# Performance work log

Hardware: AMD Instinct MI355X
Metric: run time of the kernel (lower is better)

The kernel has to match this reference:

```python
import jax, jax.numpy as jnp
import numpy as np

B, S, N, F_RAW = 32, 48, 1000, 21
H = 64           # hidden_dim
A_DIM = 10       # aspect_dim
FEAT = 4 * A_DIM # projected feature_dim = 40

OFF_IDX = np.array([2, 5, 8, 9, 12])
DEF_IDX = np.array([10, 14, 15])
ERR_IDX = np.array([13, 17])
INF_IDX = np.array([19, 20])


def _glorot(k, shape):
    lim = (6.0 / (shape[0] + shape[1])) ** 0.5
    return jax.random.uniform(k, shape, minval=-lim, maxval=lim, dtype=jnp.float32)


def setup_inputs() -> dict:
    key = jax.random.key(0)
    ks = jax.random.split(key, 12)
    return {
        'inputs': jax.random.normal(ks[0], (B, S, N, F_RAW), dtype=jnp.float32),
        'adj': jax.random.uniform(ks[1], (N, N), dtype=jnp.float32),
        # aspect projection linears (weight stored as [in, out])
        'Wo': _glorot(ks[2], (5, A_DIM)), 'bo': jnp.zeros((A_DIM,), jnp.float32),
        'Wd': _glorot(ks[3], (3, A_DIM)), 'bd': jnp.zeros((A_DIM,), jnp.float32),
        'We': _glorot(ks[4], (2, A_DIM)), 'be': jnp.zeros((A_DIM,), jnp.float32),
        'Wi': _glorot(ks[5], (2, A_DIM)), 'bi': jnp.zeros((A_DIM,), jnp.float32),
        # graph-conv GRU weights: gates (bias init 1.0) and candidate (bias 0.0)
        'W1': _glorot(ks[6], (H + FEAT, 2 * H)), 'b1': jnp.ones((2 * H,), jnp.float32),
        'W2': _glorot(ks[7], (H + FEAT, H)), 'b2': jnp.zeros((H,), jnp.float32),
    }


def _laplacian_with_self_loop(adj):
    A = adj + jnp.eye(adj.shape[0], dtype=adj.dtype)
    d_inv_sqrt = A.sum(axis=1) ** -0.5
    return d_inv_sqrt[:, None] * A * d_inv_sqrt[None, :]


def reference(inputs, adj, Wo, bo, Wd, bd, We, be, Wi, bi, W1, b1, W2, b2):
    b, s, n, _ = inputs.shape
    L = _laplacian_with_self_loop(adj)  # [N, N]

    # vectorized per-node aspect projections -> [B, S, N, 40]
    x = jnp.concatenate([
        inputs[..., OFF_IDX] @ Wo + bo,
        inputs[..., DEF_IDX] @ Wd + bd,
        inputs[..., ERR_IDX] @ We + be,
        inputs[..., INF_IDX] @ Wi + bi,
    ], axis=-1)

    def gconv(x_t, h_flat, W, bias, out_dim):
        # x_t: [B, N, FEAT]; h_flat: [B, N*H]
        cat = jnp.concatenate([x_t, h_flat.reshape(b, n, H)], axis=-1)  # [B,N,H+FEAT]
        ag = jnp.einsum('mn,bnf->bmf', L, cat)                          # [B,N,H+FEAT]
        out = ag @ W + bias                                             # [B,N,out_dim]
        return out.reshape(b, n * out_dim)

    def step(h_flat, x_t):
        # NOTE: chunk over the flattened (B, N*2H) axis, as in the torch code
        ru = jax.nn.sigmoid(gconv(x_t, h_flat, W1, b1, 2 * H))  # [B, N*2H]
        r, u = jnp.split(ru, 2, axis=1)                          # each [B, N*H]
        c = jnp.tanh(gconv(x_t, r * h_flat, W2, b2, H))          # [B, N*H]
        h_new = u * h_flat + (1.0 - u) * c
        return h_new, None

    h0 = jnp.zeros((b, n * H), dtype=inputs.dtype)
    h_last, _ = jax.lax.scan(step, h0, jnp.swapaxes(x, 0, 1))  # scan over seq
    return h_last.reshape(b, n, H)
```

## Files before the change

### kernel.cpp

```cpp
#include <hip/hip_runtime.h>
#include <math.h>

#define NN    1000
#define KP    1024
#define BATCH 32
#define SEQ   48
#define HID   64
#define LCOLS 32256

typedef unsigned short u16;
typedef __attribute__((ext_vector_type(8))) short  short8v;
typedef __attribute__((ext_vector_type(8))) unsigned short ushort8v;
typedef __attribute__((ext_vector_type(4))) float  float4v;

__device__ __forceinline__ u16 f2bf(float x) {
    union { float f; unsigned u; } v; v.f = x;
    unsigned r = v.u + 0x7FFF + ((v.u >> 16) & 1);
    return (u16)(r >> 16);
}
__device__ __forceinline__ float bf2f(u16 h) {
    union { unsigned u; float f; } v; v.u = ((unsigned)h) << 16;
    return v.f;
}

__global__ void k_rowsum(const float* __restrict__ adj, float* __restrict__ dinv) {
    int m = blockIdx.x;
    float s = 0.f;
    for (int n = threadIdx.x; n < NN; n += blockDim.x)
        s += adj[(size_t)m*NN + n];
    __shared__ float red[256];
    red[threadIdx.x] = s; __syncthreads();
    for (int st = 128; st > 0; st >>= 1) {
        if (threadIdx.x < st) red[threadIdx.x] += red[threadIdx.x + st];
        __syncthreads();
    }
    if (threadIdx.x == 0) dinv[m] = rsqrtf(red[0] + 1.0f);
}

__global__ void k_buildL(const float* __restrict__ adj, const float* __restrict__ dinv,
                         u16* __restrict__ Lhi) {
    int idx = blockIdx.x * 256 + threadIdx.x;
    if (idx >= KP*KP) return;
    int m = idx >> 10, k = idx & (KP-1);
    float v = 0.f;
    if (m < NN && k < NN)
        v = dinv[m] * (adj[(size_t)m*NN + k] + (m == k ? 1.f : 0.f)) * dinv[k];
    Lhi[idx] = f2bf(v);
}

__global__ void k_buildLf(const float* __restrict__ adj, const float* __restrict__ dinv,
                          u16* __restrict__ Lf) {
    size_t idx = (size_t)blockIdx.x * 256 + threadIdx.x;
    if (idx >= (size_t)KP*KP) return;
    int e    = idx & 7;
    int lane = (idx >> 3) & 63;
    int kb   = (idx >> 9) & 31;
    int mg   = idx >> 14;
    int m = mg*16 + (lane & 15);
    int k = kb*32 + (lane >> 4)*8 + e;
    float v = 0.f;
    if (m < NN && k < NN)
        v = dinv[m] * (adj[(size_t)m*NN + k] + (m == k ? 1.f : 0.f)) * dinv[k];
    Lf[idx] = f2bf(v);
}

__global__ void k_srow(const float* __restrict__ adj, const float* __restrict__ dinv,
                       float* __restrict__ srl) {
    int m = blockIdx.x;
    __shared__ float red[256];
    float s = 0.f;
    if (m < NN)
        for (int n = threadIdx.x; n < NN; n += blockDim.x)
            s += adj[(size_t)m*NN + n] * dinv[n];
    red[threadIdx.x] = s; __syncthreads();
    for (int st = 128; st > 0; st >>= 1) {
        if (threadIdx.x < st) red[threadIdx.x] += red[threadIdx.x + st];
        __syncthreads();
    }
    if (threadIdx.x == 0) srl[m] = (m < NN) ? dinv[m] * (red[0] + dinv[m]) : 0.f;
}

__global__ void k_wconv(const float* __restrict__ W1, const float* __restrict__ W2,
                        u16* __restrict__ W1h, u16* __restrict__ W2h) {
    int idx = blockIdx.x * 256 + threadIdx.x;
    if (idx < 128*128) {
        int k = idx >> 7, f = idx & 127;
        W1h[idx] = f2bf((f < 104) ? W1[f*128 + k] : 0.f);
    } else if (idx < 128*128 + 64*128) {
        int i2 = idx - 128*128;
        int c = i2 >> 7, f = i2 & 127;
        W2h[i2] = f2bf((f < 104) ? W2[f*64 + c] : 0.f);
    }
}

__global__ void k_packW(const float* __restrict__ Wo, const float* __restrict__ bo,
                        const float* __restrict__ Wd, const float* __restrict__ bd,
                        const float* __restrict__ We, const float* __restrict__ be,
                        const float* __restrict__ Wi, const float* __restrict__ bi,
                        float* __restrict__ Wp, float* __restrict__ bp) {
    for (int o = threadIdx.x; o < 21*40; o += 256) {
        int f = o / 40, a = o - f*40;
        int g = a / 10, aa = a - 10*g;
        float v = 0.f;
        if (g == 0) {
            if (f == 2) v = Wo[0*10+aa]; else if (f == 5) v = Wo[1*10+aa];
            else if (f == 8) v = Wo[2*10+aa]; else if (f == 9) v = Wo[3*10+aa];
            else if (f == 12) v = Wo[4*10+aa];
        } else if (g == 1) {
            if (f == 10) v = Wd[aa]; else if (f == 14) v = Wd[10+aa];
            else if (f == 15) v = Wd[20+aa];
        } else if (g == 2) {
            if (f == 13) v = We[aa]; else if (f == 17) v = We[10+aa];
        } else {
            if (f == 19) v = Wi[aa]; else if (f == 20) v = Wi[10+aa];
        }
        Wp[o] = v;
    }
    if (threadIdx.x < 40) {
        int a = threadIdx.x, g = a / 10, aa = a - 10*g;
        bp[a] = (g == 0) ? bo[aa] : (g == 1) ? bd[aa] : (g == 2) ? be[aa] : bi[aa];
    }
}

__global__ __launch_bounds__(256)
void k_transpose(const float* __restrict__ inputs, u16* __restrict__ inT) {
    int bt = blockIdx.x;
    int b = bt / SEQ, t = bt - b*SEQ;
    int nt = blockIdx.y;
    __shared__ float sm[128][22];
    const float* base = inputs + ((size_t)bt * NN + nt*128) * 21;
    for (int i = threadIdx.x; i < 128*21; i += 256) {
        int nn = i / 21, f = i - nn*21;
        int n = nt*128 + nn;
        sm[nn][f] = (n < NN) ? base[(size_t)nn*21 + f] : 0.f;
    }
    __syncthreads();
    for (int o = threadIdx.x; o < 21*128; o += 256) {
        int f = o >> 7, nn = o & 127;
        inT[(size_t)((t*32 + b)*21 + f)*KP + nt*128 + nn] = f2bf(sm[nn][f]);
    }
}

__global__ __launch_bounds__(512)
void k_gemm(const u16* __restrict__ A, const u16* __restrict__ B,
            u16* __restrict__ Cout, int ncols) {
    __shared__ char sA[128*64];
    __shared__ char sB[64*64];
    const int n0 = blockIdx.x * 64;
    const int m0 = blockIdx.y * 128;
    const int tid = threadIdx.x;
    const int w = tid >> 6, lane = tid & 63;
    const int l15 = lane & 15, l4 = lane >> 4;
    const int wm = w >> 1, wn = w & 1;

    float4v acc[2][2];
    #pragma unroll
    for (int i = 0; i < 2; ++i)
        #pragma unroll
        for (int j = 0; j < 2; ++j) acc[i][j] = (float4v){0.f,0.f,0.f,0.f};

    int aoff[2], boff[2];
    #pragma unroll
    for (int mf = 0; mf < 2; ++mf) {
        int r = wm*32 + mf*16 + l15;
        aoff[mf] = (r*64 + l4*16) ^ ((r & 7) << 4);
    }
    #pragma unroll
    for (int nf = 0; nf < 2; ++nf) {
        int r = wn*32 + nf*16 + l15;
        boff[nf] = (r*64 + l4*16) ^ ((r & 7) << 4);
    }
    const int rA = tid >> 2, qA = tid & 3;
    const int dA = (rA*64 + qA*16) ^ ((rA & 7) << 4);
    const size_t gA = (size_t)(m0 + rA)*KP + qA*8;
    const int rB = (tid & 255) >> 2, qB = tid & 3;
    const int dB = (rB*64 + qB*16) ^ ((rB & 7) << 4);
    const size_t gB = (size_t)(n0 + rB)*KP + qB*8;

    for (int kt = 0; kt < 32; ++kt) {
        const int k0 = kt*32;
        __syncthreads();
        *(uint4*)(sA + dA) = *(const uint4*)(A + gA + k0);
        if (tid < 256) *(uint4*)(sB + dB) = *(const uint4*)(B + gB + k0);
        __syncthreads();
        short8v a0 = *(const short8v*)(sA + aoff[0]);
        short8v a1 = *(const short8v*)(sA + aoff[1]);
        short8v b0 = *(const short8v*)(sB + boff[0]);
        short8v b1 = *(const short8v*)(sB + boff[1]);
        acc[0][0] = __builtin_amdgcn_mfma_f32_16x16x32_bf16(a0, b0, acc[0][0], 0, 0, 0);
        acc[0][1] = __builtin_amdgcn_mfma_f32_16x16x32_bf16(a0, b1, acc[0][1], 0, 0, 0);
        acc[1][0] = __builtin_amdgcn_mfma_f32_16x16x32_bf16(a1, b0, acc[1][0], 0, 0, 0);
        acc[1][1] = __builtin_amdgcn_mfma_f32_16x16x32_bf16(a1, b1, acc[1][1], 0, 0, 0);
    }
    #pragma unroll
    for (int mf = 0; mf < 2; ++mf)
        #pragma unroll
        for (int nf = 0; nf < 2; ++nf)
            #pragma unroll
            for (int i = 0; i < 4; ++i) {
                int m = m0 + wm*32 + mf*16 + l4*4 + i;
                int j = n0 + wn*32 + nf*16 + l15;
                Cout[(size_t)m*ncols + j] = f2bf(acc[mf][nf][i]);
            }
}

__device__ __forceinline__ size_t frag_off(int grp, int kb, int lane) {
    return (((size_t)grp*32 + kb)*64 + lane)*8;
}

__global__ __launch_bounds__(512)
void k_g1(const u16* __restrict__ Lf, const u16* __restrict__ hTf,
          const u16* __restrict__ agx, const u16* __restrict__ W1h,
          const float* __restrict__ b1, const float* __restrict__ h_lin,
          u16* __restrict__ rhf, float* __restrict__ u_lin) {
    const int b = blockIdx.x, mt = blockIdx.y;
    const int m0 = mt*64;
    const int tid = threadIdx.x;
    const int w = tid >> 6, lane = tid & 63, l15 = lane & 15, l4 = lane >> 4;
    const int wm = w >> 2, wn = w & 3;
    const int c = tid & 63, ng = tid >> 6;

    __shared__ char smem[49408];
    char* sF = smem;
    float* ru_s = (float*)(smem + 16384);

    float4v acc[2];
    acc[0] = (float4v){0.f,0.f,0.f,0.f};
    acc[1] = (float4v){0.f,0.f,0.f,0.f};
    const u16* A0 = Lf  + frag_off(mt*4 + wm*2 + 0, 0, lane);
    const u16* A1 = Lf  + frag_off(mt*4 + wm*2 + 1, 0, lane);
    const u16* B0 = hTf + frag_off(b*4  + wn, 0, lane);
    #pragma unroll 8
    for (int kb = 0; kb < 32; ++kb) {
        short8v a0 = *(const short8v*)(A0 + kb*512);
        short8v a1 = *(const short8v*)(A1 + kb*512);
        short8v b0 = *(const short8v*)(B0 + kb*512);
        acc[0] = __builtin_amdgcn_mfma_f32_16x16x32_bf16(a0, b0, acc[0], 0, 0, 0);
        acc[1] = __builtin_amdgcn_mfma_f32_16x16x32_bf16(a1, b0, acc[1], 0, 0, 0);
    }

    float hpre[2][8];
    #pragma unroll
    for (int it = 0; it < 2; ++it) {
        int nc = (it*8 + ng)*8;
        int n = 2*m0 + nc;
        if ((n >> 1) + 3 < 500) {
            #pragma unroll
            for (int d = 0; d < 8; ++d)
                hpre[it][d] = h_lin[((size_t)b*NN + n + d)*64 + c];
        }
    }

    if (tid < 192) {
        int r = tid / 3, q = tid - 3*(tid/3);
        *(uint4*)(sF + ((r*256 + (13 + q)*16) ^ ((r & 7) << 4))) = (uint4){0,0,0,0};
    }
    if (tid < 320) {
        int r = tid / 5, q = tid - 5*(tid/5);
        *(uint4*)(sF + ((r*256 + q*16) ^ ((r & 7) << 4))) =
            *(const uint4*)(agx + (size_t)(m0 + r)*1280 + b*40 + q*8);
    }
    #pragma unroll
    for (int mf = 0; mf < 2; ++mf)
        #pragma unroll
        for (int i = 0; i < 4; ++i) {
            int row = (wm*2 + mf)*16 + l4*4 + i;
            int f = 40 + wn*16 + l15;
            *(u16*)(sF + ((row*256 + f*2) ^ ((row & 7) << 4))) = f2bf(acc[mf][i]);
        }
    __syncthreads();

    const int gm = (w >> 2)*32, gn = (w & 3)*32;
    float4v acc2[2][2];
    #pragma unroll
    for (int i = 0; i < 2; ++i)
        #pragma unroll
        for (int j = 0; j < 2; ++j) acc2[i][j] = (float4v){0.f,0.f,0.f,0.f};
    for (int kt2 = 0; kt2 < 4; ++kt2) {
        #pragma unroll
        for (int mf = 0; mf < 2; ++mf) {
            int ar2 = gm + mf*16 + l15;
            short8v a = *(const short8v*)(sF + ((ar2*256 + kt2*64 + l4*16) ^ ((ar2 & 7) << 4)));
            #pragma unroll
            for (int nf = 0; nf < 2; ++nf) {
                short8v bb = *(const short8v*)(W1h + (gn + nf*16 + l15)*128 + kt2*32 + l4*8);
                acc2[mf][nf] = __builtin_amdgcn_mfma_f32_16x16x32_bf16(a, bb, acc2[mf][nf], 0, 0, 0);
            }
        }
    }
    #pragma unroll
    for (int mf = 0; mf < 2; ++mf)
        #pragma unroll
        for (int nf = 0; nf < 2; ++nf) {
            int col = gn + nf*16 + l15;
            float bias = b1[col];
            #pragma unroll
            for (int i = 0; i < 4; ++i) {
                int row = gm + mf*16 + l4*4 + i;
                ru_s[row*129 + col] = 1.f / (1.f + __expf(-(acc2[mf][nf][i] + bias)));
            }
        }
    __syncthreads();

    #pragma unroll
    for (int it = 0; it < 2; ++it) {
        int nc = (it*8 + ng)*8;
        int n = 2*m0 + nc;
        if ((n >> 1) + 3 < 500) {
            ushort8v ov;
            #pragma unroll
            for (int d = 0; d < 8; ++d) {
                int nn = n + d;
                float r = ru_s[((nc + d) >> 1)*129 + (nn & 1)*64 + c];
                ov[d] = f2bf(r * hpre[it][d]);
            }
            *(ushort8v*)(rhf + frag_off(b*4 + (c >> 4), n >> 5, (c & 15) + 16*((n >> 3) & 3))) = ov;
        }
    }
    #pragma unroll
    for (int lc = 0; lc < 8; lc += 4) {
        int lr = ng*8 + lc;
        int m = m0 + lr;
        if (m >= 500) {
            #pragma unroll
            for (int d = 0; d < 4; ++d) {
                int mm = m + d;
                if (mm < 1000) {
                    int n = 2*(mm - 500);
                    u_lin[((size_t)b*NN + n)*64 + c]     = ru_s[(lr+d)*129 + c];
                    u_lin[((size_t)b*NN + n + 1)*64 + c] = ru_s[(lr+d)*129 + 64 + c];
                }
            }
        }
    }
}

__global__ __launch_bounds__(512)
void k_g2(const u16* __restrict__ Lf, const u16* __restrict__ rhf,
          const u16* __restrict__ agx, const u16* __restrict__ W2h,
          const float* __restrict__ b2, const float* __restrict__ u_lin,
          float* __restrict__ h_lin, u16* __restrict__ hTf,
          const u16* __restrict__ LinpB, const float* __restrict__ Wp,
          const float* __restrict__ bp, const float* __restrict__ srl,
          u16* __restrict__ agx_next, int tnext,
          float* __restrict__ out, int write_out) {
    const int b = blockIdx.x, mt = blockIdx.y;
    const int m0 = mt*64;
    const int tid = threadIdx.x;
    const int w = tid >> 6, lane = tid & 63, l15 = lane & 15, l4 = lane >> 4;
    const int wm = w >> 2, wn = w & 3;
    const int c = tid & 63, ng = tid >> 6;

    __shared__ char smem[42016];
    char* sF = smem;
    float* cs  = (float*)(smem + 16384);
    float* sLp = (float*)(smem + 33024);
    float* sWp = (float*)(smem + 38656);
    __shared__ float sbp[40];
    __shared__ float ssr[64];

    float4v acc[2];
    acc[0] = (float4v){0.f,0.f,0.f,0.f};
    acc[1] = (float4v){0.f,0.f,0.f,0.f};
    const u16* A0 = Lf  + frag_off(mt*4 + wm*2 + 0, 0, lane);
    const u16* A1 = Lf  + frag_off(mt*4 + wm*2 + 1, 0, lane);
    const u16* B0 = rhf + frag_off(b*4  + wn, 0, lane);
    #pragma unroll 8
    for (int kb = 0; kb < 32; ++kb) {
        short8v a0 = *(const short8v*)(A0 + kb*512);
        short8v a1 = *(const short8v*)(A1 + kb*512);
        short8v b0 = *(const short8v*)(B0 + kb*512);
        acc[0] = __builtin_amdgcn_mfma_f32_16x16x32_bf16(a0, b0, acc[0], 0, 0, 0);
        acc[1] = __builtin_amdgcn_mfma_f32_16x16x32_bf16(a1, b0, acc[1], 0, 0, 0);
    }

    float upre[8], hpre[8];
    {
        int m = m0 + ng*8;
        #pragma unroll
        for (int d = 0; d < 8; ++d) {
            int mm = m + d;
            size_t idx = ((size_t)b*NN + mm)*64 + c;
            bool ok = mm < NN;
            upre[d] = ok ? u_lin[idx] : 0.f;
            hpre[d] = ok ? h_lin[idx] : 0.f;
        }
    }

    if (tid < 192) {
        int r = tid / 3, q = tid - 3*(tid/3);
        *(uint4*)(sF + ((r*256 + (13 + q)*16) ^ ((r & 7) << 4))) = (uint4){0,0,0,0};
    }
    if (tid < 320) {
        int r = tid / 5, q = tid - 5*(tid/5);
        *(uint4*)(sF + ((r*256 + q*16) ^ ((r & 7) << 4))) =
            *(const uint4*)(agx + (size_t)(m0 + r)*1280 + b*40 + q*8);
    }
    #pragma unroll
    for (int mf = 0; mf < 2; ++mf)
        #pragma unroll
        for (int i = 0; i < 4; ++i) {
            int row = (wm*2 + mf)*16 + l4*4 + i;
            int f = 40 + wn*16 + l15;
            *(u16*)(sF + ((row*256 + f*2) ^ ((row & 7) << 4))) = f2bf(acc[mf][i]);
        }
    __syncthreads();

    if (tnext < SEQ) {
        for (int i = tid; i < 64*21; i += 512) {
            int r = i / 21, f = i - 21*(i/21);
            sLp[r*22 + f] = bf2f(LinpB[(size_t)(m0 + r)*LCOLS + tnext*672 + b*21 + f]);
        }
        for (int i = tid; i < 21*40; i += 512) sWp[i] = Wp[i];
        if (tid < 40) sbp[tid] = bp[tid];
        if (tid < 64) ssr[tid] = srl[m0 + tid];
    }

    const int gm = (w >> 2)*32, gn = (w & 3)*16;
    float4v acc3[2];
    acc3[0] = (float4v){0.f,0.f,0.f,0.f};
    acc3[1] = (float4v){0.f,0.f,0.f,0.f};
    for (int kt2 = 0; kt2 < 4; ++kt2) {
        #pragma unroll
        for (int mf = 0; mf < 2; ++mf) {
            int ar2 = gm + mf*16 + l15;
            short8v a = *(const short8v*)(sF + ((ar2*256 + kt2*64 + l4*16) ^ ((ar2 & 7) << 4)));
            short8v bb = *(const short8v*)(W2h + (gn + l15)*128 + kt2*32 + l4*8);
            acc3[mf] = __builtin_amdgcn_mfma_f32_16x16x32_bf16(a, bb, acc3[mf], 0, 0, 0);
        }
    }
    #pragma unroll
    for (int mf = 0; mf < 2; ++mf) {
        int col = gn + l15;
        float bias = b2[col];
        #pragma unroll
        for (int i = 0; i < 4; ++i) {
            int row = gm + mf*16 + l4*4 + i;
            cs[row*65 + col] = acc3[mf][i] + bias;
        }
    }
    __syncthreads();

    {
        int lr = ng*8;
        int m = m0 + lr;
        ushort8v hiv;
        #pragma unroll
        for (int d = 0; d < 8; ++d) {
            int mm = m + d;
            float hn = 0.f;
            if (mm < NN) {
                float x = cs[(lr+d)*65 + c];
                x = fminf(fmaxf(x, -15.f), 15.f);
                float e = __expf(2.f*x);
                float cand = (e - 1.f) / (e + 1.f);
                float u = upre[d], h = hpre[d];
                hn = u*h + (1.f - u)*cand;
                size_t idx = ((size_t)b*NN + mm)*64 + c;
                h_lin[idx] = hn;
                if (write_out) out[idx] = hn;
            }
            hiv[d] = f2bf(hn);
        }
        *(ushort8v*)(hTf + frag_off(b*4 + (c >> 4), m >> 5, (c & 15) + 16*((m >> 3) & 3))) = hiv;
    }

    if (tnext < SEQ) {
        __syncthreads();
        for (int o = tid; o < 64*40; o += 512) {
            int r = o / 40, a = o - 40*(o/40);
            float acc4 = ssr[r] * sbp[a];
            #pragma unroll
            for (int f = 0; f < 21; ++f) acc4 += sLp[r*22 + f] * sWp[f*40 + a];
            agx_next[(size_t)(m0 + r)*1280 + b*40 + a] = f2bf(acc4);
        }
    }
}

__global__ __launch_bounds__(256)
void k_xproj2(const u16* __restrict__ LinpB, const float* __restrict__ Wp,
              const float* __restrict__ bp, const float* __restrict__ srl,
              u16* __restrict__ agx, int t) {
    const int b = blockIdx.x, mt = blockIdx.y;
    const int tid = threadIdx.x;
    __shared__ float sLp[64][22];
    __shared__ float sWp[21*40];
    __shared__ float sbp[40];
    __shared__ float ssr[64];
    for (int i = tid; i < 64*21; i += 256) {
        int r = i / 21, f = i - 21*(i/21);
        sLp[r][f] = bf2f(LinpB[(size_t)(mt*64 + r)*LCOLS + t*672 + b*21 + f]);
    }
    for (int i = tid; i < 21*40; i += 256) sWp[i] = Wp[i];
    if (tid < 40) sbp[tid] = bp[tid];
    if (tid < 64) ssr[tid] = srl[mt*64 + tid];
    __syncthreads();
    for (int o = tid; o < 64*40; o += 256) {
        int r = o / 40, a = o - 40*(o/40);
        float acc2 = ssr[r] * sbp[a];
        #pragma unroll
        for (int f = 0; f < 21; ++f) acc2 += sLp[r][f] * sWp[f*40 + a];
        agx[(size_t)(mt*64 + r)*1280 + b*40 + a] = f2bf(acc2);
    }
}

#define O_LHI   0ull
#define O_LF    2097152ull
#define O_LINP  4194304ull
#define O_HLIN  70254592ull
#define O_ULIN  78446592ull
#define O_HTF   86638592ull
#define O_RHF   90832896ull
#define O_AGX0  95027200ull
#define O_AGX1  97648640ull
#define O_W1H   100270080ull
#define O_W2H   100302848ull
#define O_WP    100319232ull
#define O_BP    100323328ull
#define O_DINV  100323584ull
#define O_SRL   100327680ull
#define O_INT   100331776ull

extern "C" void kernel_launch(void* const* d_in, const int* in_sizes, int n_in,
                              void* d_out, int out_size, void* d_ws, size_t ws_size,
                              hipStream_t stream) {
    const float* inputs = (const float*)d_in[0];
    const float* adj    = (const float*)d_in[1];
    const float* Wo = (const float*)d_in[2];  const float* bo = (const float*)d_in[3];
    const float* Wd = (const float*)d_in[4];  const float* bd = (const float*)d_in[5];
    const float* We = (const float*)d_in[6];  const float* be = (const float*)d_in[7];
    const float* Wi = (const float*)d_in[8];  const float* bi = (const float*)d_in[9];
    const float* W1 = (const float*)d_in[10]; const float* b1 = (const float*)d_in[11];
    const float* W2 = (const float*)d_in[12]; const float* b2 = (const float*)d_in[13];
    float* out = (float*)d_out;

    char* ws = (char*)d_ws;
    u16*   Lhi   = (u16*)(ws + O_LHI);
    u16*   Lf    = (u16*)(ws + O_LF);
    u16*   LinpB = (u16*)(ws + O_LINP);
    float* h_lin = (float*)(ws + O_HLIN);
    float* u_lin = (float*)(ws + O_ULIN);
    u16*   hTf   = (u16*)(ws + O_HTF);
    u16*   rhf   = (u16*)(ws + O_RHF);
    u16*   agx0  = (u16*)(ws + O_AGX0);
    u16*   agx1  = (u16*)(ws + O_AGX1);
    u16*   W1h   = (u16*)(ws + O_W1H);
    u16*   W2h   = (u16*)(ws + O_W2H);
    float* Wp    = (float*)(ws + O_WP);
    float* bp    = (float*)(ws + O_BP);
    float* dinv  = (float*)(ws + O_DINV);
    float* srl   = (float*)(ws + O_SRL);
    u16*   inT   = (u16*)(ws + O_INT);

    k_rowsum<<<NN, 256, 0, stream>>>(adj, dinv);
    k_buildL<<<(KP*KP)/256, 256, 0, stream>>>(adj, dinv, Lhi);
    k_buildLf<<<(KP*KP)/256, 256, 0, stream>>>(adj, dinv, Lf);
    k_srow<<<KP, 256, 0, stream>>>(adj, dinv, srl);
    k_wconv<<<96, 256, 0, stream>>>(W1, W2, W1h, W2h);
    k_packW<<<1, 256, 0, stream>>>(Wo, bo, Wd, bd, We, be, Wi, bi, Wp, bp);
    k_transpose<<<dim3(BATCH*SEQ, 8), 256, 0, stream>>>(inputs, inT);
    k_gemm<<<dim3(LCOLS/64, 8), 512, 0, stream>>>(Lhi, inT, LinpB, LCOLS);

    hipMemsetAsync(ws + O_HLIN, 0, 8192000ull, stream);
    hipMemsetAsync(ws + O_HTF,  0, 4194304ull, stream);
    hipMemsetAsync(ws + O_RHF,  0, 4194304ull, stream);
    k_xproj2<<<dim3(32,16), 256, 0, stream>>>(LinpB, Wp, bp, srl, agx0, 0);

    for (int t = 0; t < SEQ; ++t) {
        u16* agxc = (t & 1) ? agx1 : agx0;
        u16* agxn = (t & 1) ? agx0 : agx1;
        k_g1<<<dim3(32,16), 512, 0, stream>>>(Lf, hTf, agxc, W1h, b1, h_lin, rhf, u_lin);
        k_g2<<<dim3(32,16), 512, 0, stream>>>(Lf, rhf, agxc, W2h, b2, u_lin, h_lin, hTf,
                                              LinpB, Wp, bp, srl, agxn, t + 1,
                                              out, t == SEQ - 1);
    }
}
```

Measured before the change: 2.428 ms.

## Split-K the graph aggregation in GRU kernels and loop M tiles in gemm

In k_g1 and k_g2 the L×h aggregation now divides the K dimension across two halves of the warps. Each warp computes a 2x2 fragment tile over half of K, and the two halves are summed through shared memory before the bf16 store, which doubles B-fragment reuse per A load and halves the serial MFMA chain. Extra barriers are added to protect the reused shared buffers. The precompute GEMM now launches one block per N tile and loops over all eight M tiles inside, so each block handles more work but the grid has fewer blocks.

```diff
diff --git a/kernel.cpp b/kernel.cpp
--- a/kernel.cpp
+++ b/kernel.cpp
@@ -147,18 +147,11 @@
     __shared__ char sA[128*64];
     __shared__ char sB[64*64];
     const int n0 = blockIdx.x * 64;
-    const int m0 = blockIdx.y * 128;
     const int tid = threadIdx.x;
     const int w = tid >> 6, lane = tid & 63;
     const int l15 = lane & 15, l4 = lane >> 4;
     const int wm = w >> 1, wn = w & 1;
 
-    float4v acc[2][2];
-    #pragma unroll
-    for (int i = 0; i < 2; ++i)
-        #pragma unroll
-        for (int j = 0; j < 2; ++j) acc[i][j] = (float4v){0.f,0.f,0.f,0.f};
-
     int aoff[2], boff[2];
     #pragma unroll
     for (int mf = 0; mf < 2; ++mf) {
@@ -172,36 +165,46 @@
     }
     const int rA = tid >> 2, qA = tid & 3;
     const int dA = (rA*64 + qA*16) ^ ((rA & 7) << 4);
-    const size_t gA = (size_t)(m0 + rA)*KP + qA*8;
     const int rB = (tid & 255) >> 2, qB = tid & 3;
     const int dB = (rB*64 + qB*16) ^ ((rB & 7) << 4);
     const size_t gB = (size_t)(n0 + rB)*KP + qB*8;
 
-    for (int kt = 0; kt < 32; ++kt) {
-        const int k0 = kt*32;
+    for (int mt8 = 0; mt8 < 8; ++mt8) {
+        const int m0 = mt8 * 128;
+        const size_t gA = (size_t)(m0 + rA)*KP + qA*8;
+        float4v acc[2][2];
+        #pragma unroll
+        for (int i = 0; i < 2; ++i)
+            #pragma unroll
+            for (int j = 0; j < 2; ++j) acc[i][j] = (float4v){0.f,0.f,0.f,0.f};
+
+        for (int kt = 0; kt < 32; ++kt) {
+            const int k0 = kt*32;
+            __syncthreads();
+            *(uint4*)(sA + dA) = *(const uint4*)(A + gA + k0);
+            if (tid < 256) *(uint4*)(sB + dB) = *(const uint4*)(B + gB + k0);
+            __syncthreads();
+            short8v a0 = *(const short8v*)(sA + aoff[0]);
+            short8v a1 = *(const short8v*)(sA + aoff[1]);
+            short8v b0 = *(const short8v*)(sB + boff[0]);
+            short8v b1 = *(const short8v*)(sB + boff[1]);
+            acc[0][0] = __builtin_amdgcn_mfma_f32_16x16x32_bf16(a0, b0, acc[0][0], 0, 0, 0);
+            acc[0][1] = __builtin_amdgcn_mfma_f32_16x16x32_bf16(a0, b1, acc[0][1], 0, 0, 0);
+            acc[1][0] = __builtin_amdgcn_mfma_f32_16x16x32_bf16(a1, b0, acc[1][0], 0, 0, 0);
+            acc[1][1] = __builtin_amdgcn_mfma_f32_16x16x32_bf16(a1, b1, acc[1][1], 0, 0, 0);
+        }
+        #pragma unroll
+        for (int mf = 0; mf < 2; ++mf)
+            #pragma unroll
+            for (int nf = 0; nf < 2; ++nf)
+                #pragma unroll
+                for (int i = 0; i < 4; ++i) {
+                    int m = m0 + wm*32 + mf*16 + l4*4 + i;
+                    int j = n0 + wn*32 + nf*16 + l15;
+                    Cout[(size_t)m*ncols + j] = f2bf(acc[mf][nf][i]);
+                }
         __syncthreads();
-        *(uint4*)(sA + dA) = *(const uint4*)(A + gA + k0);
-        if (tid < 256) *(uint4*)(sB + dB) = *(const uint4*)(B + gB + k0);
-        __syncthreads();
-        short8v a0 = *(const short8v*)(sA + aoff[0]);
-        short8v a1 = *(const short8v*)(sA + aoff[1]);
-        short8v b0 = *(const short8v*)(sB + boff[0]);
-        short8v b1 = *(const short8v*)(sB + boff[1]);
-        acc[0][0] = __builtin_amdgcn_mfma_f32_16x16x32_bf16(a0, b0, acc[0][0], 0, 0, 0);
-        acc[0][1] = __builtin_amdgcn_mfma_f32_16x16x32_bf16(a0, b1, acc[0][1], 0, 0, 0);
-        acc[1][0] = __builtin_amdgcn_mfma_f32_16x16x32_bf16(a1, b0, acc[1][0], 0, 0, 0);
-        acc[1][1] = __builtin_amdgcn_mfma_f32_16x16x32_bf16(a1, b1, acc[1][1], 0, 0, 0);
-    }
-    #pragma unroll
-    for (int mf = 0; mf < 2; ++mf)
-        #pragma unroll
-        for (int nf = 0; nf < 2; ++nf)
-            #pragma unroll
-            for (int i = 0; i < 4; ++i) {
-                int m = m0 + wm*32 + mf*16 + l4*4 + i;
-                int j = n0 + wn*32 + nf*16 + l15;
-                Cout[(size_t)m*ncols + j] = f2bf(acc[mf][nf][i]);
-            }
+    }
 }
 
 __device__ __forceinline__ size_t frag_off(int grp, int kb, int lane) {
@@ -217,26 +220,32 @@
     const int m0 = mt*64;
     const int tid = threadIdx.x;
     const int w = tid >> 6, lane = tid & 63, l15 = lane & 15, l4 = lane >> 4;
-    const int wm = w >> 2, wn = w & 3;
+    const int kh = w >> 2, q = w & 3, qi = q >> 1, qj = q & 1;
     const int c = tid & 63, ng = tid >> 6;
 
     __shared__ char smem[49408];
     char* sF = smem;
     float* ru_s = (float*)(smem + 16384);
 
-    float4v acc[2];
-    acc[0] = (float4v){0.f,0.f,0.f,0.f};
-    acc[1] = (float4v){0.f,0.f,0.f,0.f};
-    const u16* A0 = Lf  + frag_off(mt*4 + wm*2 + 0, 0, lane);
-    const u16* A1 = Lf  + frag_off(mt*4 + wm*2 + 1, 0, lane);
-    const u16* B0 = hTf + frag_off(b*4  + wn, 0, lane);
+    float4v acc[2][2];
+    #pragma unroll
+    for (int i = 0; i < 2; ++i)
+        #pragma unroll
+        for (int j = 0; j < 2; ++j) acc[i][j] = (float4v){0.f,0.f,0.f,0.f};
+    const u16* A0 = Lf  + frag_off(mt*4 + qi*2 + 0, kh*16, lane);
+    const u16* A1 = Lf  + frag_off(mt*4 + qi*2 + 1, kh*16, lane);
+    const u16* B0 = hTf + frag_off(b*4  + qj*2 + 0, kh*16, lane);
+    const u16* B1 = hTf + frag_off(b*4  + qj*2 + 1, kh*16, lane);
     #pragma unroll 8
-    for (int kb = 0; kb < 32; ++kb) {
+    for (int kb = 0; kb < 16; ++kb) {
         short8v a0 = *(const short8v*)(A0 + kb*512);
         short8v a1 = *(const short8v*)(A1 + kb*512);
         short8v b0 = *(const short8v*)(B0 + kb*512);
-        acc[0] = __builtin_amdgcn_mfma_f32_16x16x32_bf16(a0, b0, acc[0], 0, 0, 0);
-        acc[1] = __builtin_amdgcn_mfma_f32_16x16x32_bf16(a1, b0, acc[1], 0, 0, 0);
+        short8v b1 = *(const short8v*)(B1 + kb*512);
+        acc[0][0] = __builtin_amdgcn_mfma_f32_16x16x32_bf16(a0, b0, acc[0][0], 0, 0, 0);
+        acc[0][1] = __builtin_amdgcn_mfma_f32_16x16x32_bf16(a0, b1, acc[0][1], 0, 0, 0);
+        acc[1][0] = __builtin_amdgcn_mfma_f32_16x16x32_bf16(a1, b0, acc[1][0], 0, 0, 0);
+        acc[1][1] = __builtin_amdgcn_mfma_f32_16x16x32_bf16(a1, b1, acc[1][1], 0, 0, 0);
     }
 
     float hpre[2][8];
@@ -251,23 +260,37 @@
         }
     }
 
+    float* red = ru_s;
+    if (kh == 1) {
+        #pragma unroll
+        for (int fr = 0; fr < 4; ++fr)
+            *(float4v*)(red + (((size_t)q*4 + fr)*64 + lane)*4) = acc[fr>>1][fr&1];
+    }
     if (tid < 192) {
-        int r = tid / 3, q = tid - 3*(tid/3);
-        *(uint4*)(sF + ((r*256 + (13 + q)*16) ^ ((r & 7) << 4))) = (uint4){0,0,0,0};
+        int r = tid / 3, qq = tid - 3*(tid/3);
+        *(uint4*)(sF + ((r*256 + (13 + qq)*16) ^ ((r & 7) << 4))) = (uint4){0,0,0,0};
     }
     if (tid < 320) {
-        int r = tid / 5, q = tid - 5*(tid/5);
-        *(uint4*)(sF + ((r*256 + q*16) ^ ((r & 7) << 4))) =
-            *(const uint4*)(agx + (size_t)(m0 + r)*1280 + b*40 + q*8);
-    }
-    #pragma unroll
-    for (int mf = 0; mf < 2; ++mf)
-        #pragma unroll
-        for (int i = 0; i < 4; ++i) {
-            int row = (wm*2 + mf)*16 + l4*4 + i;
-            int f = 40 + wn*16 + l15;
-            *(u16*)(sF + ((row*256 + f*2) ^ ((row & 7) << 4))) = f2bf(acc[mf][i]);
-        }
+        int r = tid / 5, qq = tid - 5*(tid/5);
+        *(uint4*)(sF + ((r*256 + qq*16) ^ ((r & 7) << 4))) =
+            *(const uint4*)(agx + (size_t)(m0 + r)*1280 + b*40 + qq*8);
+    }
+    __syncthreads();
+    if (kh == 0) {
+        #pragma unroll
+        for (int fr = 0; fr < 4; ++fr)
+            acc[fr>>1][fr&1] += *(const float4v*)(red + (((size_t)q*4 + fr)*64 + lane)*4);
+        #pragma unroll
+        for (int mf = 0; mf < 2; ++mf)
+            #pragma unroll
+            for (int nf = 0; nf < 2; ++nf)
+                #pragma unroll
+                for (int i = 0; i < 4; ++i) {
+                    int row = (qi*2 + mf)*16 + l4*4 + i;
+                    int f = 40 + (qj*2 + nf)*16 + l15;
+                    *(u16*)(sF + ((row*256 + f*2) ^ ((row & 7) << 4))) = f2bf(acc[mf][nf][i]);
+                }
+    }
     __syncthreads();
 
     const int gm = (w >> 2)*32, gn = (w & 3)*32;
@@ -288,6 +311,7 @@
             }
         }
     }
+    __syncthreads();
     #pragma unroll
     for (int mf = 0; mf < 2; ++mf)
         #pragma unroll
@@ -348,7 +372,7 @@
     const int m0 = mt*64;
     const int tid = threadIdx.x;
     const int w = tid >> 6, lane = tid & 63, l15 = lane & 15, l4 = lane >> 4;
-    const int wm = w >> 2, wn = w & 3;
+    const int kh = w >> 2, q = w & 3, qi = q >> 1, qj = q & 1;
     const int c = tid & 63, ng = tid >> 6;
 
     __shared__ char smem[42016];
@@ -359,19 +383,25 @@
     __shared__ float sbp[40];
     __shared__ float ssr[64];
 
-    float4v acc[2];
-    acc[0] = (float4v){0.f,0.f,0.f,0.f};
-    acc[1] = (float4v){0.f,0.f,0.f,0.f};
-    const u16* A0 = Lf  + frag_off(mt*4 + wm*2 + 0, 0, lane);
-    const u16* A1 = Lf  + frag_off(mt*4 + wm*2 + 1, 0, lane);
-    const u16* B0 = rhf + frag_off(b*4  + wn, 0, lane);
+    float4v acc[2][2];
+    #pragma unroll
+    for (int i = 0; i < 2; ++i)
+        #pragma unroll
+        for (int j = 0; j < 2; ++j) acc[i][j] = (float4v){0.f,0.f,0.f,0.f};
+    const u16* A0 = Lf  + frag_off(mt*4 + qi*2 + 0, kh*16, lane);
+    const u16* A1 = Lf  + frag_off(mt*4 + qi*2 + 1, kh*16, lane);
+    const u16* B0 = rhf + frag_off(b*4  + qj*2 + 0, kh*16, lane);
+    const u16* B1 = rhf + frag_off(b*4  + qj*2 + 1, kh*16, lane);
     #pragma unroll 8
-    for (int kb = 0; kb < 32; ++kb) {
+    for (int kb = 0; kb < 16; ++kb) {
         short8v a0 = *(const short8v*)(A0 + kb*512);
         short8v a1 = *(const short8v*)(A1 + kb*512);
         short8v b0 = *(const short8v*)(B0 + kb*512);
-        acc[0] = __builtin_amdgcn_mfma_f32_16x16x32_bf16(a0, b0, acc[0], 0, 0, 0);
-        acc[1] = __builtin_amdgcn_mfma_f32_16x16x32_bf16(a1, b0, acc[1], 0, 0, 0);
+        short8v b1 = *(const short8v*)(B1 + kb*512);
+        acc[0][0] = __builtin_amdgcn_mfma_f32_16x16x32_bf16(a0, b0, acc[0][0], 0, 0, 0);
+        acc[0][1] = __builtin_amdgcn_mfma_f32_16x16x32_bf16(a0, b1, acc[0][1], 0, 0, 0);
+        acc[1][0] = __builtin_amdgcn_mfma_f32_16x16x32_bf16(a1, b0, acc[1][0], 0, 0, 0);
+        acc[1][1] = __builtin_amdgcn_mfma_f32_16x16x32_bf16(a1, b1, acc[1][1], 0, 0, 0);
     }
 
     float upre[8], hpre[8];
@@ -387,23 +417,37 @@
         }
     }
 
+    float* red = cs;
+    if (kh == 1) {
+        #pragma unroll
+        for (int fr = 0; fr < 4; ++fr)
+            *(float4v*)(red + (((size_t)q*4 + fr)*64 + lane)*4) = acc[fr>>1][fr&1];
+    }
     if (tid < 192) {
-        int r = tid / 3, q = tid - 3*(tid/3);
-        *(uint4*)(sF + ((r*256 + (13 + q)*16) ^ ((r & 7) << 4))) = (uint4){0,0,0,0};
+        int r = tid / 3, qq = tid - 3*(tid/3);
+        *(uint4*)(sF + ((r*256 + (13 + qq)*16) ^ ((r & 7) << 4))) = (uint4){0,0,0,0};
     }
     if (tid < 320) {
-        int r = tid / 5, q = tid - 5*(tid/5);
-        *(uint4*)(sF + ((r*256 + q*16) ^ ((r & 7) << 4))) =
-            *(const uint4*)(agx + (size_t)(m0 + r)*1280 + b*40 + q*8);
-    }
-    #pragma unroll
-    for (int mf = 0; mf < 2; ++mf)
-        #pragma unroll
-        for (int i = 0; i < 4; ++i) {
-            int row = (wm*2 + mf)*16 + l4*4 + i;
-            int f = 40 + wn*16 + l15;
-            *(u16*)(sF + ((row*256 + f*2) ^ ((row & 7) << 4))) = f2bf(acc[mf][i]);
-        }
+        int r = tid / 5, qq = tid - 5*(tid/5);
+        *(uint4*)(sF + ((r*256 + qq*16) ^ ((r & 7) << 4))) =
+            *(const uint4*)(agx + (size_t)(m0 + r)*1280 + b*40 + qq*8);
+    }
+    __syncthreads();
+    if (kh == 0) {
+        #pragma unroll
+        for (int fr = 0; fr < 4; ++fr)
+            acc[fr>>1][fr&1] += *(const float4v*)(red + (((size_t)q*4 + fr)*64 + lane)*4);
+        #pragma unroll
+        for (int mf = 0; mf < 2; ++mf)
+            #pragma unroll
+            for (int nf = 0; nf < 2; ++nf)
+                #pragma unroll
+                for (int i = 0; i < 4; ++i) {
+                    int row = (qi*2 + mf)*16 + l4*4 + i;
+                    int f = 40 + (qj*2 + nf)*16 + l15;
+                    *(u16*)(sF + ((row*256 + f*2) ^ ((row & 7) << 4))) = f2bf(acc[mf][nf][i]);
+                }
+    }
     __syncthreads();
 
     if (tnext < SEQ) {
@@ -429,6 +473,7 @@
             acc3[mf] = __builtin_amdgcn_mfma_f32_16x16x32_bf16(a, bb, acc3[mf], 0, 0, 0);
         }
     }
+    __syncthreads();
     #pragma unroll
     for (int mf = 0; mf < 2; ++mf) {
         int col = gn + l15;
@@ -559,7 +604,7 @@
     k_wconv<<<96, 256, 0, stream>>>(W1, W2, W1h, W2h);
     k_packW<<<1, 256, 0, stream>>>(Wo, bo, Wd, bd, We, be, Wi, bi, Wp, bp);
     k_transpose<<<dim3(BATCH*SEQ, 8), 256, 0, stream>>>(inputs, inT);
-    k_gemm<<<dim3(LCOLS/64, 8), 512, 0, stream>>>(Lhi, inT, LinpB, LCOLS);
+    k_gemm<<<dim3(LCOLS/64), 512, 0, stream>>>(Lhi, inT, LinpB, LCOLS);
 
     hipMemsetAsync(ws + O_HLIN, 0, 8192000ull, stream);
     hipMemsetAsync(ws + O_HTF,  0, 4194304ull, stream);
```

After: 2.238 ms. 7.8% less time.
